# Kernel tuning notes

Measured on AMD Instinct MI355X. Metric: run time of the kernel, lower is better.

## Reference

```python
import jax, jax.numpy as jnp
import numpy as np

B, L_SRC, L_TGT, H = 8, 256, 256, 768
N_SRC_WORDS, N_TGT_WORDS = 128, 128


def setup_inputs() -> dict:
    key = jax.random.key(0)
    k1, k2 = jax.random.split(key, 2)
    L = L_SRC + L_TGT
    tok_h = jax.random.normal(k1, (B, L, H), dtype=jnp.float32)
    attention_mask = jnp.ones((B, L), dtype=jnp.int32)
    # monotone word ids covering exactly N words (ragged spans of ~2 tokens/word)
    src_ids = (jnp.arange(L_SRC) * N_SRC_WORDS // L_SRC).astype(jnp.int64)
    tgt_ids = (jnp.arange(L_TGT) * N_TGT_WORDS // L_TGT).astype(jnp.int64)
    source_word_ids = jnp.broadcast_to(src_ids, (B, L_SRC))
    target_word_ids = jnp.broadcast_to(tgt_ids, (B, L_TGT))
    W = jax.random.normal(k2, (2 * H, 1), dtype=jnp.float32) * 0.02
    b = jnp.zeros((1,), dtype=jnp.float32)
    return dict(tok_h=tok_h, attention_mask=attention_mask,
                source_word_ids=source_word_ids, target_word_ids=target_word_ids,
                W=W, b=b, S=N_SRC_WORDS, T=N_TGT_WORDS)


def _pool_words(tok_h, combined_wid, attention_mask, n_words):
    """Vectorized equivalent of _pool_word_embeddings: mean over each
    contiguous run of equal word ids (masked / -1 tokens break runs)."""
    Bv, Lv, Hv = tok_h.shape
    valid = (attention_mask > 0) & (combined_wid >= 0)          # [B, L]
    prev_wid = jnp.pad(combined_wid[:, :-1], ((0, 0), (1, 0)), constant_values=-2)
    prev_valid = jnp.pad(valid[:, :-1], ((0, 0), (1, 0)), constant_values=False)
    new_run = valid & ((combined_wid != prev_wid) | (~prev_valid))
    run_id = jnp.cumsum(new_run.astype(jnp.int32), axis=1) - 1  # [B, L]
    n_seg = n_words + 1                                         # +1 dummy slot for invalid tokens
    seg = jnp.where(valid, run_id, n_words)
    gseg = (seg + jnp.arange(Bv, dtype=seg.dtype)[:, None] * n_seg).reshape(-1)
    sums = jax.ops.segment_sum(tok_h.reshape(Bv * Lv, Hv), gseg,
                               num_segments=Bv * n_seg).reshape(Bv, n_seg, Hv)
    counts = jax.ops.segment_sum(valid.astype(tok_h.dtype).reshape(-1), gseg,
                                 num_segments=Bv * n_seg).reshape(Bv, n_seg, 1)
    pooled = sums[:, :n_words] / jnp.maximum(counts[:, :n_words], 1.0)
    return pooled                                               # [B, n_words, H]


def reference(tok_h, attention_mask, source_word_ids, target_word_ids, W, b, S, T):
    combined_wid = jnp.concatenate([source_word_ids, target_word_ids], axis=1)  # [B, L]
    pooled = _pool_words(tok_h, combined_wid, attention_mask, S + T)            # [B, S+T, H]
    src = pooled[:, :S]            # [B, S, H]
    tgt = pooled[:, S:S + T]       # [B, T, H]
    # classifier(concat([src_exp, tgt_exp])) == src@W[:H] + tgt@W[H:] + b
    Hd = tok_h.shape[-1]
    w_src, w_tgt = W[:Hd, 0], W[Hd:, 0]
    logits = (src @ w_src)[:, :, None] + (tgt @ w_tgt)[:, None, :] + b[0]       # [B, S, T]
    return logits
```

## Files before the change

### kernel.cpp

```cpp
#include <hip/hip_runtime.h>
#include <hip/hip_bf16.h>

constexpr int B  = 8;
constexpr int LS = 256;
constexpr int L  = 512;
constexpr int H  = 768;
constexpr int S  = 128;
constexpr int NW = 256;

__global__ __launch_bounds__(256) void dot2_kernel(
    const float* __restrict__ tok, const float* __restrict__ Wp,
    float2* __restrict__ dvals)
{
    const int lane = threadIdx.x & 63;
    const int wv   = threadIdx.x >> 6;
    const int t0   = (blockIdx.x * 4 + wv) * 4;

    const float4* s4 = reinterpret_cast<const float4*>(Wp);
    const float4* g4 = reinterpret_cast<const float4*>(Wp + H);
    float4 wsv[3], wtv[3];
    #pragma unroll
    for (int k = 0; k < 3; ++k) {
        wsv[k] = s4[lane + 64 * k];
        wtv[k] = g4[lane + 64 * k];
    }

    #pragma unroll
    for (int t = 0; t < 4; ++t) {
        const float4* t4 = reinterpret_cast<const float4*>(tok + (size_t)(t0 + t) * H);
        float as = 0.f, at = 0.f;
        #pragma unroll
        for (int k = 0; k < 3; ++k) {
            const float4 a = t4[lane + 64 * k];
            as += a.x * wsv[k].x + a.y * wsv[k].y + a.z * wsv[k].z + a.w * wsv[k].w;
            at += a.x * wtv[k].x + a.y * wtv[k].y + a.z * wtv[k].z + a.w * wtv[k].w;
        }
        #pragma unroll
        for (int off = 32; off; off >>= 1) {
            as += __shfl_xor(as, off);
            at += __shfl_xor(at, off);
        }
        if (lane == 0) dvals[t0 + t] = make_float2(as, at);
    }
}

__global__ __launch_bounds__(256) void finalize_kernel(
    const int* __restrict__ mask, const int* __restrict__ sw,
    const int* __restrict__ tw, const float2* __restrict__ dvals,
    const float* __restrict__ bias, float* __restrict__ out)
{
    const int g   = blockIdx.x;
    const int b   = g >> 3;
    const int s   = g & 7;
    const int tid = threadIdx.x;

    __shared__ int   sseg[L];
    __shared__ float lsum[NW + 1];
    __shared__ float lcnt[NW + 1];
    __shared__ float pooled[NW];

    if (tid < NW + 1) { lsum[tid] = 0.f; lcnt[tid] = 0.f; }
    __syncthreads();

    if (tid < 64) {
        const int lane = tid;
        const int base = lane * 8;
        int wid[8]; bool val[8];
        #pragma unroll
        for (int j = 0; j < 8; ++j) {
            const int l = base + j;
            const int w = (l < LS) ? sw[b * LS + l] : tw[b * LS + (l - LS)];
            wid[j] = w;
            val[j] = (mask[b * L + l] > 0) && (w >= 0);
        }
        int pw = -2; bool pv = false;
        if (base > 0) {
            const int l = base - 1;
            pw = (l < LS) ? sw[b * LS + l] : tw[b * LS + (l - LS)];
            pv = (mask[b * L + l] > 0) && (pw >= 0);
        }
        int loc[8]; int c = 0;
        #pragma unroll
        for (int j = 0; j < 8; ++j) {
            const int nr = (val[j] && (wid[j] != pw || !pv)) ? 1 : 0;
            c += nr; loc[j] = c; pw = wid[j]; pv = val[j];
        }
        int inc = c;
        #pragma unroll
        for (int off = 1; off < 64; off <<= 1) {
            const int v = __shfl_up(inc, off);
            if (lane >= off) inc += v;
        }
        const int excl = inc - c;
        #pragma unroll
        for (int j = 0; j < 8; ++j) {
            const int rid = excl + loc[j] - 1;
            const int sg  = (val[j] && rid < NW) ? rid : NW;
            sseg[base + j] = sg;
            atomicAdd(&lcnt[sg], 1.0f);
        }
    }
    __syncthreads();

    #pragma unroll
    for (int r = 0; r < 2; ++r) {
        const int tl = tid + r * 256;
        const int sg = sseg[tl];
        if (sg < NW) {
            const float2 d = dvals[b * L + tl];
            atomicAdd(&lsum[sg], (sg < S) ? d.x : d.y);
        }
    }
    __syncthreads();

    if (tid < NW) pooled[tid] = lsum[tid] / fmaxf(lcnt[tid], 1.f);
    __syncthreads();

    const float b0 = bias[0];
    const int r = s * 16 + (tid >> 4);
    const int c = (tid & 15) * 8;
    const float si = pooled[r] + b0;

    float4* o = reinterpret_cast<float4*>(out + (size_t)b * S * 128 + r * 128 + c);
    #pragma unroll
    for (int j = 0; j < 8; j += 4) {
        float4 v;
        v.x = si + pooled[S + c + j + 0];
        v.y = si + pooled[S + c + j + 1];
        v.z = si + pooled[S + c + j + 2];
        v.w = si + pooled[S + c + j + 3];
        o[j >> 2] = v;
    }
}

extern "C" void kernel_launch(void* const* d_in, const int* in_sizes, int n_in,
                              void* d_out, int out_size, void* d_ws, size_t ws_size,
                              hipStream_t stream) {
    const float* tok  = (const float*)d_in[0];
    const int*   mask = (const int*)  d_in[1];
    const int*   sw   = (const int*)  d_in[2];
    const int*   tw   = (const int*)  d_in[3];
    const float* W    = (const float*)d_in[4];
    const float* bias = (const float*)d_in[5];
    float*       out  = (float*)d_out;

    float2* dvals = (float2*)d_ws;

    dot2_kernel<<<256, 256, 0, stream>>>(tok, W, dvals);
    finalize_kernel<<<64, 256, 0, stream>>>(mask, sw, tw, dvals, bias, out);
}
```

Before: 14.31 us.

## Fuse dot-product and pooling kernels with inter-block flag synchronization

```diff
diff --git a/kernel.cpp b/kernel.cpp
--- a/kernel.cpp
+++ b/kernel.cpp
@@ -7,52 +7,59 @@
 constexpr int H  = 768;
 constexpr int S  = 128;
 constexpr int NW = 256;
+constexpr unsigned TAG = 0x7C1A55EDu;
 
-__global__ __launch_bounds__(256) void dot2_kernel(
-    const float* __restrict__ tok, const float* __restrict__ Wp,
-    float2* __restrict__ dvals)
+__global__ __launch_bounds__(256) void fused_kernel(
+    const float* __restrict__ tok, const int* __restrict__ mask,
+    const int* __restrict__ sw, const int* __restrict__ tw,
+    const float* __restrict__ Wp, const float* __restrict__ bias,
+    float* __restrict__ out, float2* __restrict__ dvals,
+    unsigned* __restrict__ flags)
 {
-    const int lane = threadIdx.x & 63;
-    const int wv   = threadIdx.x >> 6;
-    const int t0   = (blockIdx.x * 4 + wv) * 4;
+    const int g    = blockIdx.x;
+    const int tid  = threadIdx.x;
+    const int lane = tid & 63;
+    const int wv   = tid >> 6;
 
-    const float4* s4 = reinterpret_cast<const float4*>(Wp);
-    const float4* g4 = reinterpret_cast<const float4*>(Wp + H);
-    float4 wsv[3], wtv[3];
-    #pragma unroll
-    for (int k = 0; k < 3; ++k) {
-        wsv[k] = s4[lane + 64 * k];
-        wtv[k] = g4[lane + 64 * k];
+    {
+        const float4* s4 = reinterpret_cast<const float4*>(Wp);
+        const float4* g4 = reinterpret_cast<const float4*>(Wp + H);
+        float4 wsv[3], wtv[3];
+        #pragma unroll
+        for (int k = 0; k < 3; ++k) {
+            wsv[k] = s4[lane + 64 * k];
+            wtv[k] = g4[lane + 64 * k];
+        }
+        const int t0 = g * 16 + wv * 4;
+        #pragma unroll
+        for (int t = 0; t < 4; ++t) {
+            const float4* t4 = reinterpret_cast<const float4*>(tok + (size_t)(t0 + t) * H);
+            float as = 0.f, at = 0.f;
+            #pragma unroll
+            for (int k = 0; k < 3; ++k) {
+                const float4 a = t4[lane + 64 * k];
+                as += a.x * wsv[k].x + a.y * wsv[k].y + a.z * wsv[k].z + a.w * wsv[k].w;
+                at += a.x * wtv[k].x + a.y * wtv[k].y + a.z * wtv[k].z + a.w * wtv[k].w;
+            }
+            #pragma unroll
+            for (int off = 32; off; off >>= 1) {
+                as += __shfl_xor(as, off);
+                at += __shfl_xor(at, off);
+            }
+            if (lane == 0) dvals[t0 + t] = make_float2(as, at);
+        }
+    }
+    __syncthreads();
+    if (tid == 0) {
+        __threadfence();
+        __hip_atomic_store(&flags[g], TAG, __ATOMIC_RELEASE,
+                           __HIP_MEMORY_SCOPE_AGENT);
     }
 
-    #pragma unroll
-    for (int t = 0; t < 4; ++t) {
-        const float4* t4 = reinterpret_cast<const float4*>(tok + (size_t)(t0 + t) * H);
-        float as = 0.f, at = 0.f;
-        #pragma unroll
-        for (int k = 0; k < 3; ++k) {
-            const float4 a = t4[lane + 64 * k];
-            as += a.x * wsv[k].x + a.y * wsv[k].y + a.z * wsv[k].z + a.w * wsv[k].w;
-            at += a.x * wtv[k].x + a.y * wtv[k].y + a.z * wtv[k].z + a.w * wtv[k].w;
-        }
-        #pragma unroll
-        for (int off = 32; off; off >>= 1) {
-            as += __shfl_xor(as, off);
-            at += __shfl_xor(at, off);
-        }
-        if (lane == 0) dvals[t0 + t] = make_float2(as, at);
-    }
-}
+    if (g >= 64) return;
 
-__global__ __launch_bounds__(256) void finalize_kernel(
-    const int* __restrict__ mask, const int* __restrict__ sw,
-    const int* __restrict__ tw, const float2* __restrict__ dvals,
-    const float* __restrict__ bias, float* __restrict__ out)
-{
-    const int g   = blockIdx.x;
-    const int b   = g >> 3;
-    const int s   = g & 7;
-    const int tid = threadIdx.x;
+    const int b  = g >> 3;
+    const int sl = g & 7;
 
     __shared__ int   sseg[L];
     __shared__ float lsum[NW + 1];
@@ -62,8 +69,7 @@
     if (tid < NW + 1) { lsum[tid] = 0.f; lcnt[tid] = 0.f; }
     __syncthreads();
 
-    if (tid < 64) {
-        const int lane = tid;
+    if (wv == 0) {
         const int base = lane * 8;
         int wid[8]; bool val[8];
         #pragma unroll
@@ -99,6 +105,11 @@
             sseg[base + j] = sg;
             atomicAdd(&lcnt[sg], 1.0f);
         }
+    } else if (wv == 1 && lane < 32) {
+        while (__hip_atomic_load(&flags[b * 32 + lane], __ATOMIC_ACQUIRE,
+                                 __HIP_MEMORY_SCOPE_AGENT) != TAG) {
+            __builtin_amdgcn_s_sleep(1);
+        }
     }
     __syncthreads();
 
@@ -117,7 +128,7 @@
     __syncthreads();
 
     const float b0 = bias[0];
-    const int r = s * 16 + (tid >> 4);
+    const int r = sl * 16 + (tid >> 4);
     const int c = (tid & 15) * 8;
     const float si = pooled[r] + b0;
 
@@ -144,8 +155,9 @@
     const float* bias = (const float*)d_in[5];
     float*       out  = (float*)d_out;
 
-    float2* dvals = (float2*)d_ws;
+    float2*   dvals = (float2*)d_ws;
+    unsigned* flags = (unsigned*)(dvals + B * L);
 
-    dot2_kernel<<<256, 256, 0, stream>>>(tok, W, dvals);
-    finalize_kernel<<<64, 256, 0, stream>>>(mask, sw, tw, dvals, bias, out);
+    fused_kernel<<<256, 256, 0, stream>>>(tok, mask, sw, tw, W, bias,
+                                          out, dvals, flags);
 }
```

New measurement: 18.81 us. 1.31x slower.
